# Kernel tuning notes

Hardware: AMD Instinct MI355X
Metric: run time of the kernel (lower is better)

## Reference

```python
import jax, jax.numpy as jnp
import numpy as np

N = 100000   # nodes
E = 1600000  # edges (avg degree 16)
D = 64       # din == dout
L = 4        # n_layers
EPS = 1e-5   # pyg LayerNorm eps


def setup_inputs() -> dict:
    key = jax.random.key(0)
    k = jax.random.split(key, 4)
    x = jax.random.normal(k[0], (N, D), dtype=jnp.float32)
    edge_index = jax.random.randint(k[1], (2, E), 0, N, dtype=jnp.int32)
    Ws = jax.random.normal(k[2], (L, D, D), dtype=jnp.float32) * (1.0 / np.sqrt(D))
    bs = jnp.zeros((L, D), dtype=jnp.float32)
    ln_w = jnp.ones((L, D), dtype=jnp.float32)
    ln_b = jnp.zeros((L, D), dtype=jnp.float32)
    return {"x": x, "edge_index": edge_index, "Ws": Ws, "bs": bs, "ln_w": ln_w, "ln_b": ln_b}


def reference(x, edge_index, Ws, bs, ln_w, ln_b):
    src, dst = edge_index[0], edge_index[1]
    n = x.shape[0]
    # GCN symmetric normalization with self-loops: deg = 1 + in-degree
    deg = jnp.zeros((n,), x.dtype).at[dst].add(1.0) + 1.0
    dinv = jax.lax.rsqrt(deg)                       # [N]
    enorm = (dinv[src] * dinv[dst])[:, None]        # [E,1]
    self_norm = (dinv * dinv)[:, None]              # [N,1]

    h = x
    for l in range(Ws.shape[0]):
        hw = h @ Ws[l]                              # [N,D]
        # gather-normalize-scatter neighborhood aggregation + self-loop term
        agg = jnp.zeros_like(hw).at[dst].add(enorm * hw[src])
        agg = agg + self_norm * hw + bs[l]
        # pyg LayerNorm (mode='graph', batch=None): mean/var over all nodes+channels
        mean = jnp.mean(agg)
        var = jnp.mean(jnp.square(agg - mean))
        hn = ln_w[l] * (agg - mean) * jax.lax.rsqrt(var + EPS) + ln_b[l]
        h = jax.nn.relu(hn)                         # dropout p=0.0 -> identity
    return h
```

## Files before the change

### kernel.cpp

```cpp
#include <hip/hip_runtime.h>

#define DD 64
#define NBUCK 256
#define BSTRIDE 32
#define CAP 13312
#define GSTRIDE 16
#define TILE 4096

__device__ __forceinline__ unsigned pack_bf16_2(float a, float b) {
  unsigned ua = __float_as_uint(a);
  unsigned ub = __float_as_uint(b);
  unsigned ra = (ua + 0x7FFFu + ((ua >> 16) & 1u)) >> 16;
  unsigned rb = (ub + 0x7FFFu + ((ub >> 16) & 1u)) >> 16;
  return ra | (rb << 16);
}

__device__ __forceinline__ float4 unpack_bf16_4(uint2 p) {
  float4 f;
  f.x = __uint_as_float(p.x << 16);
  f.y = __uint_as_float(p.x & 0xFFFF0000u);
  f.z = __uint_as_float(p.y << 16);
  f.w = __uint_as_float(p.y & 0xFFFF0000u);
  return f;
}

__device__ __forceinline__ void ln_stats(const double* __restrict__ buckets, int M,
                                         float* mean_out, float* rstd_out) {
  __shared__ double ra[4], rb[4];
  __shared__ float sm[2];
  int t = threadIdx.x;
  double a = buckets[(size_t)t * BSTRIDE];
  double b = buckets[(size_t)t * BSTRIDE + 1];
#pragma unroll
  for (int o = 1; o <= 32; o <<= 1) {
    a += __shfl_xor(a, o);
    b += __shfl_xor(b, o);
  }
  if ((t & 63) == 0) { ra[t >> 6] = a; rb[t >> 6] = b; }
  __syncthreads();
  if (t == 0) {
    double s1 = ra[0] + ra[1] + ra[2] + ra[3];
    double s2 = rb[0] + rb[1] + rb[2] + rb[3];
    double mean = s1 / M;
    double var = s2 / M - mean * mean;
    sm[0] = (float)mean;
    sm[1] = (float)rsqrt(var + 1e-5);
  }
  __syncthreads();
  *mean_out = sm[0];
  *rstd_out = sm[1];
}


__global__ __launch_bounds__(256) void init_gcur_k(int* __restrict__ gcur, int nbkt) {
  int t = blockIdx.x * 256 + threadIdx.x;
  if (t < nbkt) gcur[t * GSTRIDE] = t * CAP;
}

__global__ __launch_bounds__(256) void bucket_a_k(const int* __restrict__ src, const int* __restrict__ dst,
                                                  int* __restrict__ gcur, unsigned* __restrict__ slots, int E) {
  __shared__ int hist[256], cur[256], hbase[256];
  int t = threadIdx.x;
  hist[t] = 0;
  cur[t] = 0;
  __syncthreads();
  int t0 = blockIdx.x * TILE;
  unsigned pk[16];
  int bk[16];
#pragma unroll
  for (int k = 0; k < 16; ++k) {
    int e = t0 + k * 256 + t;
    if (e < E) {
      int s = src[e], d = dst[e];
      bk[k] = d >> 9;
      pk[k] = (unsigned)s | ((unsigned)(d & 511) << 17);
      atomicAdd(&hist[bk[k]], 1);
    } else {
      bk[k] = -1;
      pk[k] = 0;
    }
  }
  __syncthreads();
  if (hist[t] > 0) hbase[t] = atomicAdd(&gcur[t * GSTRIDE], hist[t]);
  __syncthreads();
#pragma unroll
  for (int k = 0; k < 16; ++k) {
    if (bk[k] >= 0) {
      int r = atomicAdd(&cur[bk[k]], 1);
      slots[(size_t)hbase[bk[k]] + r] = pk[k];
    }
  }
}

__global__ __launch_bounds__(256) void scan_nb_k(const int* __restrict__ gcur, int* __restrict__ bbase, int nbkt) {
  __shared__ int ts[256];
  int t = threadIdx.x;
  int c = (t < nbkt) ? (gcur[t * GSTRIDE] - t * CAP) : 0;
  ts[t] = c;
  __syncthreads();
  for (int o = 1; o < 256; o <<= 1) {
    int u = (t >= o) ? ts[t - o] : 0;
    __syncthreads();
    ts[t] += u;
    __syncthreads();
  }
  if (t < nbkt) bbase[t] = ts[t] - c;
}

__global__ __launch_bounds__(256) void bucket_b_k(const unsigned* __restrict__ slots,
                                                  const int* __restrict__ gcur, const int* __restrict__ bbase,
                                                  int* __restrict__ offv, float* __restrict__ dinv,
                                                  int* __restrict__ csr, int N, int E) {
  __shared__ int hist[512], excl[512], ts[256];
  int b = blockIdx.x, t = threadIdx.x;
  int base = b * CAP;
  int cnt = gcur[b * GSTRIDE] - base;
  if (cnt > CAP) cnt = CAP;
  int cbase = bbase[b];
  int node0 = b << 9;
  hist[t] = 0;
  hist[t + 256] = 0;
  __syncthreads();
  for (int i = t; i < cnt; i += 256) atomicAdd(&hist[slots[(size_t)base + i] >> 17], 1);
  __syncthreads();
  int h0 = hist[2 * t], h1 = hist[2 * t + 1];
  int pair = h0 + h1;
  ts[t] = pair;
  __syncthreads();
  for (int o = 1; o < 256; o <<= 1) {
    int u = (t >= o) ? ts[t - o] : 0;
    __syncthreads();
    ts[t] += u;
    __syncthreads();
  }
  int ep = ts[t] - pair;
  int j0 = node0 + 2 * t, j1 = j0 + 1;
  if (j0 < N) { offv[j0] = cbase + ep; dinv[j0] = rsqrtf((float)h0 + 1.0f); }
  if (j1 < N) { offv[j1] = cbase + ep + h0; dinv[j1] = rsqrtf((float)h1 + 1.0f); }
  if (b == (int)gridDim.x - 1 && t == 0) offv[N] = E;
  excl[2 * t] = cbase + ep;
  excl[2 * t + 1] = cbase + ep + h0;
  __syncthreads();
  for (int i = t; i < cnt; i += 256) {
    unsigned e = slots[(size_t)base + i];
    int pos = atomicAdd(&excl[e >> 17], 1);
    csr[pos] = (int)(e & 0x1FFFFu);
  }
}


__global__ __launch_bounds__(256) void gemm_ln_k(const float* __restrict__ in, const float* __restrict__ W,
                                                 uint4* __restrict__ hwb, const float* __restrict__ dinv,
                                                 const float* __restrict__ lnw, const float* __restrict__ lnb,
                                                 const double* __restrict__ buckets, int M,
                                                 int applyLn, int n) {
  __shared__ float Wl[64 * 64];
  __shared__ float Al[64 * 68];
  int t = threadIdx.x;
  float mean = 0.f, rstd = 1.f;
  if (applyLn) ln_stats(buckets, M, &mean, &rstd);
#pragma unroll
  for (int i = 0; i < 4; ++i)
    ((float4*)Wl)[t + i * 256] = ((const float4*)W)[t + i * 256];
  int row0 = blockIdx.x * 64;
#pragma unroll
  for (int i = 0; i < 4; ++i) {
    int q = t + i * 256;
    int r = q >> 4, c4 = q & 15;
    int gr = row0 + r;
    float4 v = make_float4(0.f, 0.f, 0.f, 0.f);
    if (gr < n) v = ((const float4*)in)[(size_t)gr * 16 + c4];
    if (applyLn) {
      int c = c4 * 4;
      v.x = fmaxf(fmaf((v.x - mean) * rstd, lnw[c + 0], lnb[c + 0]), 0.f);
      v.y = fmaxf(fmaf((v.y - mean) * rstd, lnw[c + 1], lnb[c + 1]), 0.f);
      v.z = fmaxf(fmaf((v.z - mean) * rstd, lnw[c + 2], lnb[c + 2]), 0.f);
      v.w = fmaxf(fmaf((v.w - mean) * rstd, lnw[c + 3], lnb[c + 3]), 0.f);
    }
    *(float4*)&Al[r * 68 + c4 * 4] = v;
  }
  __syncthreads();
  int r = t >> 2, cb = (t & 3) * 16;
  float acc[16];
#pragma unroll
  for (int j = 0; j < 16; ++j) acc[j] = 0.f;
  for (int k = 0; k < 64; ++k) {
    float a = Al[r * 68 + k];
#pragma unroll
    for (int j = 0; j < 16; ++j) acc[j] = fmaf(a, Wl[k * 64 + cb + j], acc[j]);
  }
  int gr = row0 + r;
  if (gr < n) {
    float di = dinv[gr];
#pragma unroll
    for (int j = 0; j < 16; ++j) acc[j] *= di;
    uint4 u0, u1;
    u0.x = pack_bf16_2(acc[0], acc[1]);
    u0.y = pack_bf16_2(acc[2], acc[3]);
    u0.z = pack_bf16_2(acc[4], acc[5]);
    u0.w = pack_bf16_2(acc[6], acc[7]);
    u1.x = pack_bf16_2(acc[8], acc[9]);
    u1.y = pack_bf16_2(acc[10], acc[11]);
    u1.z = pack_bf16_2(acc[12], acc[13]);
    u1.w = pack_bf16_2(acc[14], acc[15]);
    hwb[(size_t)gr * 8 + (t & 3) * 2 + 0] = u0;
    hwb[(size_t)gr * 8 + (t & 3) * 2 + 1] = u1;
  }
}

__global__ __launch_bounds__(256) void agg_k(const uint2* __restrict__ hwb, const int* __restrict__ off,
                                             const int* __restrict__ csr, const float* __restrict__ dinv,
                                             const float4* __restrict__ bias4, float4* __restrict__ out4,
                                             double* __restrict__ buckets, int n) {
  int wid = (int)((blockIdx.x * 256 + threadIdx.x) >> 6);
  int lane = threadIdx.x & 63;
  int g = lane >> 4, q = lane & 15;
  float4 acc = make_float4(0.f, 0.f, 0.f, 0.f);
  float s1 = 0.f, s2 = 0.f;
  if (wid < n) {
    if (g == 0) {
      acc = unpack_bf16_4(hwb[(size_t)wid * 16 + q]);
    }
    int e0 = off[wid], e1 = off[wid + 1];
    for (int base = e0; base < e1; base += 16) {
      int eb = base + g * 4;
      int c0 = csr[eb + 0];
      int c1 = csr[eb + 1];
      int c2 = csr[eb + 2];
      int c3 = csr[eb + 3];
      int i0 = (eb + 0 < e1) ? c0 : 0;
      int i1 = (eb + 1 < e1) ? c1 : 0;
      int i2 = (eb + 2 < e1) ? c2 : 0;
      int i3 = (eb + 3 < e1) ? c3 : 0;
      float w0 = (eb + 0 < e1) ? 1.f : 0.f;
      float w1 = (eb + 1 < e1) ? 1.f : 0.f;
      float w2 = (eb + 2 < e1) ? 1.f : 0.f;
      float w3 = (eb + 3 < e1) ? 1.f : 0.f;
      float4 v0 = unpack_bf16_4(hwb[(size_t)i0 * 16 + q]);
      float4 v1 = unpack_bf16_4(hwb[(size_t)i1 * 16 + q]);
      float4 v2 = unpack_bf16_4(hwb[(size_t)i2 * 16 + q]);
      float4 v3 = unpack_bf16_4(hwb[(size_t)i3 * 16 + q]);
      acc.x = fmaf(w0, v0.x, acc.x); acc.y = fmaf(w0, v0.y, acc.y);
      acc.z = fmaf(w0, v0.z, acc.z); acc.w = fmaf(w0, v0.w, acc.w);
      acc.x = fmaf(w1, v1.x, acc.x); acc.y = fmaf(w1, v1.y, acc.y);
      acc.z = fmaf(w1, v1.z, acc.z); acc.w = fmaf(w1, v1.w, acc.w);
      acc.x = fmaf(w2, v2.x, acc.x); acc.y = fmaf(w2, v2.y, acc.y);
      acc.z = fmaf(w2, v2.z, acc.z); acc.w = fmaf(w2, v2.w, acc.w);
      acc.x = fmaf(w3, v3.x, acc.x); acc.y = fmaf(w3, v3.y, acc.y);
      acc.z = fmaf(w3, v3.z, acc.z); acc.w = fmaf(w3, v3.w, acc.w);
    }
#pragma unroll
    for (int o = 16; o <= 32; o <<= 1) {
      acc.x += __shfl_xor(acc.x, o);
      acc.y += __shfl_xor(acc.y, o);
      acc.z += __shfl_xor(acc.z, o);
      acc.w += __shfl_xor(acc.w, o);
    }
    if (g == 0) {
      float dd = dinv[wid];
      float4 b = bias4[q];
      acc.x = fmaf(dd, acc.x, b.x);
      acc.y = fmaf(dd, acc.y, b.y);
      acc.z = fmaf(dd, acc.z, b.z);
      acc.w = fmaf(dd, acc.w, b.w);
      out4[(size_t)wid * 16 + q] = acc;
      s1 = acc.x + acc.y + acc.z + acc.w;
      s2 = acc.x * acc.x + acc.y * acc.y + acc.z * acc.z + acc.w * acc.w;
    }
  }
#pragma unroll
  for (int o = 1; o <= 32; o <<= 1) {
    s1 += __shfl_xor(s1, o);
    s2 += __shfl_xor(s2, o);
  }
  __shared__ float red1[4], red2[4];
  int w = threadIdx.x >> 6;
  if (lane == 0) { red1[w] = s1; red2[w] = s2; }
  __syncthreads();
  if (threadIdx.x == 0) {
    double a = (double)red1[0] + (double)red1[1] + (double)red1[2] + (double)red1[3];
    double b = (double)red2[0] + (double)red2[1] + (double)red2[2] + (double)red2[3];
    double* bp = buckets + (size_t)(blockIdx.x & (NBUCK - 1)) * BSTRIDE;
    atomicAdd(&bp[0], a);
    atomicAdd(&bp[1], b);
  }
}

__global__ __launch_bounds__(256) void norm_relu_k(float4* __restrict__ io, const float* __restrict__ lnw,
                                                   const float* __restrict__ lnb,
                                                   const double* __restrict__ buckets, int M, int n4) {
  float mean, rstd;
  ln_stats(buckets, M, &mean, &rstd);
  for (int i = blockIdx.x * 256 + threadIdx.x; i < n4; i += gridDim.x * 256) {
    float4 v = io[i];
    int c = (i & 15) * 4;
    v.x = fmaxf(fmaf((v.x - mean) * rstd, lnw[c + 0], lnb[c + 0]), 0.f);
    v.y = fmaxf(fmaf((v.y - mean) * rstd, lnw[c + 1], lnb[c + 1]), 0.f);
    v.z = fmaxf(fmaf((v.z - mean) * rstd, lnw[c + 2], lnb[c + 2]), 0.f);
    v.w = fmaxf(fmaf((v.w - mean) * rstd, lnw[c + 3], lnb[c + 3]), 0.f);
    io[i] = v;
  }
}


extern "C" void kernel_launch(void* const* d_in, const int* in_sizes, int n_in,
                              void* d_out, int out_size, void* d_ws, size_t ws_size,
                              hipStream_t stream) {
  const float* x = (const float*)d_in[0];
  const int* ei = (const int*)d_in[1];
  const float* Ws = (const float*)d_in[2];
  const float* bs = (const float*)d_in[3];
  const float* lnw = (const float*)d_in[4];
  const float* lnb = (const float*)d_in[5];
  float* out = (float*)d_out;

  const int N = in_sizes[0] / DD;
  const int E = in_sizes[1] / 2;
  const int L = in_sizes[2] / (DD * DD);
  const int* srcp = ei;
  const int* dstp = ei + E;
  const int nbkt = (N + 511) >> 9;

  char* p = (char*)d_ws;
  size_t ofs = 0;
  auto carve = [&](size_t bytes) -> void* {
    void* r = p + ofs;
    ofs = (ofs + bytes + 255) & ~(size_t)255;
    return r;
  };
  int* gcur = (int*)carve((size_t)256 * GSTRIDE * 4);
  int* bbase = (int*)carve((size_t)256 * 4);
  unsigned* slots = (unsigned*)carve((size_t)256 * CAP * 4);
  double* buckets = (double*)carve((size_t)NBUCK * BSTRIDE * 8 * 4);
  int* offv = (int*)carve((size_t)(N + 1) * 4);
  float* dinv = (float*)carve((size_t)N * 4);
  int* csr = (int*)carve((size_t)(E + 16) * 4);
  uint4* hwb = (uint4*)carve((size_t)N * DD * 2);

  hipMemsetAsync(buckets, 0, (size_t)NBUCK * BSTRIDE * 8 * 4, stream);

  init_gcur_k<<<1, 256, 0, stream>>>(gcur, nbkt);
  int nTiles = (E + TILE - 1) / TILE;
  bucket_a_k<<<nTiles, 256, 0, stream>>>(srcp, dstp, gcur, slots, E);
  scan_nb_k<<<1, 256, 0, stream>>>(gcur, bbase, nbkt);
  bucket_b_k<<<nbkt, 256, 0, stream>>>(slots, gcur, bbase, offv, dinv, csr, N, E);

  int gGemm = (N + 63) / 64;
  int gAgg = (N * DD + 255) / 256;
  for (int l = 0; l < L; ++l) {
    const float* in = (l == 0) ? x : out;
    const float* plnw = (l == 0) ? lnw : lnw + (l - 1) * DD;
    const float* plnb = (l == 0) ? lnb : lnb + (l - 1) * DD;
    const double* pbuck = buckets + (size_t)((l == 0) ? 0 : (l - 1)) * NBUCK * BSTRIDE;
    gemm_ln_k<<<gGemm, 256, 0, stream>>>(in, Ws + (size_t)l * DD * DD, hwb, dinv, plnw, plnb,
                                         pbuck, N * DD, (l > 0) ? 1 : 0, N);
    double* lbuck = buckets + (size_t)l * NBUCK * BSTRIDE;
    agg_k<<<gAgg, 256, 0, stream>>>((const uint2*)hwb, offv, csr, dinv,
                                    (const float4*)(bs + (size_t)l * DD), (float4*)out,
                                    lbuck, N);
  }
  norm_relu_k<<<1024, 256, 0, stream>>>((float4*)out, lnw + (size_t)(L - 1) * DD,
                                        lnb + (size_t)(L - 1) * DD,
                                        buckets + (size_t)(L - 1) * NBUCK * BSTRIDE,
                                        N * DD, N * (DD / 4));
}
```

Before: 375.3 us.

## Pad CSR rows to 16 with sentinel node and batch 8 nodes per wavefront

Each node's CSR segment is padded to a multiple of 16 entries and the padding points to a zeroed sentinel row in the bf16 feature buffer. This lets the aggregation loop use aligned int4 index loads with no bounds checks or masks. Each wavefront now handles 8 nodes in sequence, so the per-block reduction and atomic traffic drop and far fewer blocks are launched. The cost is extra padded gather traffic on the zero row, a larger CSR buffer with per-bucket slack, and fewer blocks available to hide memory latency.

```diff
diff --git a/kernel.cpp b/kernel.cpp
--- a/kernel.cpp
+++ b/kernel.cpp
@@ -6,6 +6,7 @@
 #define CAP 13312
 #define GSTRIDE 16
 #define TILE 4096
+#define BSLACK 8192
 
 __device__ __forceinline__ unsigned pack_bf16_2(float a, float b) {
   unsigned ua = __float_as_uint(a);
@@ -109,14 +110,14 @@
 
 __global__ __launch_bounds__(256) void bucket_b_k(const unsigned* __restrict__ slots,
                                                   const int* __restrict__ gcur, const int* __restrict__ bbase,
-                                                  int* __restrict__ offv, float* __restrict__ dinv,
-                                                  int* __restrict__ csr, int N, int E) {
+                                                  int2* __restrict__ off2, float* __restrict__ dinv,
+                                                  int* __restrict__ csr, int N) {
   __shared__ int hist[512], excl[512], ts[256];
   int b = blockIdx.x, t = threadIdx.x;
   int base = b * CAP;
   int cnt = gcur[b * GSTRIDE] - base;
   if (cnt > CAP) cnt = CAP;
-  int cbase = bbase[b];
+  int cbase = bbase[b] + b * BSLACK;
   int node0 = b << 9;
   hist[t] = 0;
   hist[t + 256] = 0;
@@ -124,7 +125,8 @@
   for (int i = t; i < cnt; i += 256) atomicAdd(&hist[slots[(size_t)base + i] >> 17], 1);
   __syncthreads();
   int h0 = hist[2 * t], h1 = hist[2 * t + 1];
-  int pair = h0 + h1;
+  int p0 = (h0 + 15) & ~15, p1 = (h1 + 15) & ~15;
+  int pair = p0 + p1;
   ts[t] = pair;
   __syncthreads();
   for (int o = 1; o < 256; o <<= 1) {
@@ -134,18 +136,21 @@
     __syncthreads();
   }
   int ep = ts[t] - pair;
+  int start0 = cbase + ep, start1 = cbase + ep + p0;
   int j0 = node0 + 2 * t, j1 = j0 + 1;
-  if (j0 < N) { offv[j0] = cbase + ep; dinv[j0] = rsqrtf((float)h0 + 1.0f); }
-  if (j1 < N) { offv[j1] = cbase + ep + h0; dinv[j1] = rsqrtf((float)h1 + 1.0f); }
-  if (b == (int)gridDim.x - 1 && t == 0) offv[N] = E;
-  excl[2 * t] = cbase + ep;
-  excl[2 * t + 1] = cbase + ep + h0;
+  if (j0 < N) { off2[j0] = make_int2(start0, start0 + p0); dinv[j0] = rsqrtf((float)h0 + 1.0f); }
+  if (j1 < N) { off2[j1] = make_int2(start1, start1 + p1); dinv[j1] = rsqrtf((float)h1 + 1.0f); }
+  excl[2 * t] = start0;
+  excl[2 * t + 1] = start1;
   __syncthreads();
   for (int i = t; i < cnt; i += 256) {
     unsigned e = slots[(size_t)base + i];
     int pos = atomicAdd(&excl[e >> 17], 1);
     csr[pos] = (int)(e & 0x1FFFFu);
   }
+  __syncthreads();
+  for (int i = h0; i < p0; ++i) csr[start0 + i] = N;
+  for (int i = h1; i < p1; ++i) csr[start1 + i] = N;
 }
 
 
@@ -208,46 +213,37 @@
   }
 }
 
-__global__ __launch_bounds__(256) void agg_k(const uint2* __restrict__ hwb, const int* __restrict__ off,
+__global__ __launch_bounds__(256) void agg_k(const uint2* __restrict__ hwb, const int2* __restrict__ off2,
                                              const int* __restrict__ csr, const float* __restrict__ dinv,
                                              const float4* __restrict__ bias4, float4* __restrict__ out4,
                                              double* __restrict__ buckets, int n) {
-  int wid = (int)((blockIdx.x * 256 + threadIdx.x) >> 6);
-  int lane = threadIdx.x & 63;
+  int t = threadIdx.x;
+  int lane = t & 63;
+  int w = t >> 6;
   int g = lane >> 4, q = lane & 15;
-  float4 acc = make_float4(0.f, 0.f, 0.f, 0.f);
+  int wbase = (blockIdx.x * 4 + w) * 8;
   float s1 = 0.f, s2 = 0.f;
-  if (wid < n) {
-    if (g == 0) {
-      acc = unpack_bf16_4(hwb[(size_t)wid * 16 + q]);
-    }
-    int e0 = off[wid], e1 = off[wid + 1];
-    for (int base = e0; base < e1; base += 16) {
-      int eb = base + g * 4;
-      int c0 = csr[eb + 0];
-      int c1 = csr[eb + 1];
-      int c2 = csr[eb + 2];
-      int c3 = csr[eb + 3];
-      int i0 = (eb + 0 < e1) ? c0 : 0;
-      int i1 = (eb + 1 < e1) ? c1 : 0;
-      int i2 = (eb + 2 < e1) ? c2 : 0;
-      int i3 = (eb + 3 < e1) ? c3 : 0;
-      float w0 = (eb + 0 < e1) ? 1.f : 0.f;
-      float w1 = (eb + 1 < e1) ? 1.f : 0.f;
-      float w2 = (eb + 2 < e1) ? 1.f : 0.f;
-      float w3 = (eb + 3 < e1) ? 1.f : 0.f;
-      float4 v0 = unpack_bf16_4(hwb[(size_t)i0 * 16 + q]);
-      float4 v1 = unpack_bf16_4(hwb[(size_t)i1 * 16 + q]);
-      float4 v2 = unpack_bf16_4(hwb[(size_t)i2 * 16 + q]);
-      float4 v3 = unpack_bf16_4(hwb[(size_t)i3 * 16 + q]);
-      acc.x = fmaf(w0, v0.x, acc.x); acc.y = fmaf(w0, v0.y, acc.y);
-      acc.z = fmaf(w0, v0.z, acc.z); acc.w = fmaf(w0, v0.w, acc.w);
-      acc.x = fmaf(w1, v1.x, acc.x); acc.y = fmaf(w1, v1.y, acc.y);
-      acc.z = fmaf(w1, v1.z, acc.z); acc.w = fmaf(w1, v1.w, acc.w);
-      acc.x = fmaf(w2, v2.x, acc.x); acc.y = fmaf(w2, v2.y, acc.y);
-      acc.z = fmaf(w2, v2.z, acc.z); acc.w = fmaf(w2, v2.w, acc.w);
-      acc.x = fmaf(w3, v3.x, acc.x); acc.y = fmaf(w3, v3.y, acc.y);
-      acc.z = fmaf(w3, v3.z, acc.z); acc.w = fmaf(w3, v3.w, acc.w);
+#pragma unroll 1
+  for (int ni = 0; ni < 8; ++ni) {
+    int wid = wbase + ni;
+    if (wid >= n) break;
+    int2 oo = off2[wid];
+    float4 acc = make_float4(0.f, 0.f, 0.f, 0.f);
+    if (g == 0) acc = unpack_bf16_4(hwb[(size_t)wid * 16 + q]);
+    for (int base = oo.x; base < oo.y; base += 16) {
+      int4 c = *(const int4*)(csr + base + g * 4);
+      float4 v0 = unpack_bf16_4(hwb[(size_t)c.x * 16 + q]);
+      float4 v1 = unpack_bf16_4(hwb[(size_t)c.y * 16 + q]);
+      float4 v2 = unpack_bf16_4(hwb[(size_t)c.z * 16 + q]);
+      float4 v3 = unpack_bf16_4(hwb[(size_t)c.w * 16 + q]);
+      float ax = v0.x + v1.x, bx = v2.x + v3.x;
+      float ay = v0.y + v1.y, by = v2.y + v3.y;
+      float az = v0.z + v1.z, bz = v2.z + v3.z;
+      float aw = v0.w + v1.w, bw = v2.w + v3.w;
+      acc.x += ax + bx;
+      acc.y += ay + by;
+      acc.z += az + bz;
+      acc.w += aw + bw;
     }
 #pragma unroll
     for (int o = 16; o <= 32; o <<= 1) {
@@ -264,8 +260,8 @@
       acc.z = fmaf(dd, acc.z, b.z);
       acc.w = fmaf(dd, acc.w, b.w);
       out4[(size_t)wid * 16 + q] = acc;
-      s1 = acc.x + acc.y + acc.z + acc.w;
-      s2 = acc.x * acc.x + acc.y * acc.y + acc.z * acc.z + acc.w * acc.w;
+      s1 += acc.x + acc.y + acc.z + acc.w;
+      s2 += acc.x * acc.x + acc.y * acc.y + acc.z * acc.z + acc.w * acc.w;
     }
   }
 #pragma unroll
@@ -274,10 +270,9 @@
     s2 += __shfl_xor(s2, o);
   }
   __shared__ float red1[4], red2[4];
-  int w = threadIdx.x >> 6;
   if (lane == 0) { red1[w] = s1; red2[w] = s2; }
   __syncthreads();
-  if (threadIdx.x == 0) {
+  if (t == 0) {
     double a = (double)red1[0] + (double)red1[1] + (double)red1[2] + (double)red1[3];
     double b = (double)red2[0] + (double)red2[1] + (double)red2[2] + (double)red2[3];
     double* bp = buckets + (size_t)(blockIdx.x & (NBUCK - 1)) * BSTRIDE;
@@ -332,21 +327,22 @@
   int* bbase = (int*)carve((size_t)256 * 4);
   unsigned* slots = (unsigned*)carve((size_t)256 * CAP * 4);
   double* buckets = (double*)carve((size_t)NBUCK * BSTRIDE * 8 * 4);
-  int* offv = (int*)carve((size_t)(N + 1) * 4);
+  int2* off2 = (int2*)carve((size_t)N * 8);
   float* dinv = (float*)carve((size_t)N * 4);
-  int* csr = (int*)carve((size_t)(E + 16) * 4);
-  uint4* hwb = (uint4*)carve((size_t)N * DD * 2);
+  int* csr = (int*)carve(((size_t)E + (size_t)nbkt * BSLACK + 64) * 4);
+  uint4* hwb = (uint4*)carve((size_t)(N + 1) * DD * 2);
 
   hipMemsetAsync(buckets, 0, (size_t)NBUCK * BSTRIDE * 8 * 4, stream);
+  hipMemsetAsync(hwb + (size_t)N * 8, 0, DD * 2, stream);
 
   init_gcur_k<<<1, 256, 0, stream>>>(gcur, nbkt);
   int nTiles = (E + TILE - 1) / TILE;
   bucket_a_k<<<nTiles, 256, 0, stream>>>(srcp, dstp, gcur, slots, E);
   scan_nb_k<<<1, 256, 0, stream>>>(gcur, bbase, nbkt);
-  bucket_b_k<<<nbkt, 256, 0, stream>>>(slots, gcur, bbase, offv, dinv, csr, N, E);
+  bucket_b_k<<<nbkt, 256, 0, stream>>>(slots, gcur, bbase, off2, dinv, csr, N);
 
   int gGemm = (N + 63) / 64;
-  int gAgg = (N * DD + 255) / 256;
+  int gAgg = (N + 31) / 32;
   for (int l = 0; l < L; ++l) {
     const float* in = (l == 0) ? x : out;
     const float* plnw = (l == 0) ? lnw : lnw + (l - 1) * DD;
@@ -355,7 +351,7 @@
     gemm_ln_k<<<gGemm, 256, 0, stream>>>(in, Ws + (size_t)l * DD * DD, hwb, dinv, plnw, plnb,
                                          pbuck, N * DD, (l > 0) ? 1 : 0, N);
     double* lbuck = buckets + (size_t)l * NBUCK * BSTRIDE;
-    agg_k<<<gAgg, 256, 0, stream>>>((const uint2*)hwb, offv, csr, dinv,
+    agg_k<<<gAgg, 256, 0, stream>>>((const uint2*)hwb, off2, csr, dinv,
                                     (const float4*)(bs + (size_t)l * DD), (float4*)out,
                                     lbuck, N);
   }
```

Result: faster. 360.5 us (-3.9%).
